# Kernel optimization log

Measured on AMD Instinct MI355X. Metric: run time of the kernel, lower is better.

The kernel has to match this reference:

```python
import jax, jax.numpy as jnp
import numpy as np
import math

EMBED_DIM = 128
SCALE = math.sqrt(EMBED_DIM)


def setup_inputs() -> dict:
    key = jax.random.key(0)
    # x: [B, N, D, L] = [4, 16, 128, 2048]
    x = jax.random.normal(key, (4, 16, 128, 2048), dtype=jnp.float32)
    return {"x": x}


def reference(x):
    # x: [B, N, D, L] -> [B, N, L, D]
    xt = jnp.swapaxes(x, -1, -2)
    # scores: [B, N, L, L] = softmax(x x^T / sqrt(D))
    scores = jnp.einsum("bnld,bnmd->bnlm", xt, xt) / jnp.asarray(SCALE, xt.dtype)
    attn = jax.nn.softmax(scores, axis=-1)
    # weighted values then mean over query positions L -> [B, N, D]
    out = jnp.einsum("bnlm,bnmd->bnld", attn, xt).mean(axis=2)
    return out
```

## Files before the change

### kernel.cpp

```cpp
#include <hip/hip_runtime.h>
#include <hip/hip_fp16.h>

#define H_  64
#define D_  128
#define L_  2048
#define RSCALE 0.08838834764831845f

typedef _Float16 half8 __attribute__((ext_vector_type(8)));
typedef float    f32x4 __attribute__((ext_vector_type(4)));

__device__ __forceinline__ void gload16(const void* g, void* l) {
    __builtin_amdgcn_global_load_lds(
        (const __attribute__((address_space(1))) void*)g,
        (__attribute__((address_space(3))) void*)l,
        16, 0, 0);
}

template <int NSW>
__device__ __forceinline__ void stage_tile(const char* __restrict__ src,
                                           char* __restrict__ dst,
                                           int wid, int lane) {
#pragma unroll
    for (int j = 0; j < NSW; ++j) {
        const unsigned o   = (unsigned)(wid * NSW + j) * 1024u + (unsigned)lane * 16u;
        const unsigned row = o >> 8;
        const unsigned so  = (o & ~255u) | ((o & 255u) ^ ((row & 7u) << 4));
        gload16(src + so, dst + (size_t)(wid * NSW + j) * 1024u);
    }
}

__global__ __launch_bounds__(256) void k_transpose(const float* __restrict__ x,
                                                   __half* __restrict__ xt) {
    const int h  = blockIdx.x;
    const int lc = blockIdx.y;
    __shared__ float raw[128][65];
    const float* xh = x + (size_t)h * D_ * L_ + (size_t)lc * 64;
    const int t = threadIdx.x;
    const int r0 = t >> 4;
    const int c4 = (t & 15) << 2;
#pragma unroll
    for (int i = 0; i < 8; ++i) {
        const int d = i * 16 + r0;
        const float4 v = *(const float4*)(xh + (size_t)d * L_ + c4);
        raw[d][c4 + 0] = v.x; raw[d][c4 + 1] = v.y;
        raw[d][c4 + 2] = v.z; raw[d][c4 + 3] = v.w;
    }
    __syncthreads();
    const int lane = t & 63, w = t >> 6;
    __half2* xth = (__half2*)(xt + (size_t)h * L_ * D_ + (size_t)lc * 64 * D_);
#pragma unroll
    for (int i = 0; i < 16; ++i) {
        const int jl = w * 16 + i;
        const float a = raw[2 * lane][jl];
        const float b = raw[2 * lane + 1][jl];
        xth[(size_t)jl * 64 + lane] = __floats2half2_rn(a, b);
    }
}

template <int PASS>
__global__ __launch_bounds__(512, 2) void k_gemm(const __half* __restrict__ xt,
                                                 const float* __restrict__ ainv,
                                                 float* __restrict__ zw) {
    __shared__ char  smA[65536];
    __shared__ char  smB[2][32768];
    __shared__ float csum[2][4][128];
    __shared__ float zfin[2][256];

    const int bid = blockIdx.x;
    const int xq  = bid >> 3;
    const int pid = xq & 3;
    const int h   = ((xq >> 2) << 3) | (bid & 7);
    const int SLOTS = (PASS == 1) ? 9 : 10;

    const int t    = threadIdx.x;
    const int lane = t & 63;
    const int wid  = t >> 6;
    const int wr   = wid >> 1;
    const int wc   = wid & 1;
    const int lo   = lane & 15, hi = lane >> 4;
    const unsigned sx = (unsigned)((lane & 7) << 4);

    const char* xh = (const char*)(xt + (size_t)h * (L_ * D_));
    float* zwh = zw + (((size_t)h * SLOTS) << 11);

#pragma unroll 1
    for (int pp = 0; pp < 2; ++pp) {
        const int p     = pp ? (7 - pid) : pid;
        const int nst   = 16 - 2 * p;
        const int rtile = 2 * p + (wr >> 1);

        stage_tile<8>(xh + (size_t)(2 * p) * 32768, smA, wid, lane);
        stage_tile<4>(xh + (size_t)(2 * p) * 32768, smB[0], wid, lane);

        float rs[4][4] = {};
        float ar[4][4];
        if (PASS == 2) {
#pragma unroll
            for (int fm = 0; fm < 4; ++fm)
#pragma unroll
                for (int r = 0; r < 4; ++r)
                    ar[fm][r] = ainv[((size_t)h << 11) + p * 256 + wr * 64 + fm * 16 + hi * 4 + r];
        }
        __syncthreads();

#pragma unroll 1
        for (int it = 0; it < nst; ++it) {
            const int ct = 2 * p + it;
            if (it + 1 < nst)
                stage_tile<4>(xh + (size_t)(ct + 1) * 32768, smB[(it + 1) & 1], wid, lane);

            float acol[4];
            if (PASS == 2) {
#pragma unroll
                for (int fn = 0; fn < 4; ++fn)
                    acol[fn] = ainv[((size_t)h << 11) + ct * 128 + wc * 64 + fn * 16 + lo];
            }

            const int rel = ct - rtile;
            float cs[4] = {0.f, 0.f, 0.f, 0.f};
            if (rel >= 0) {
                f32x4 acc[4][4] = {};
                const char* tb = smB[it & 1];
#pragma unroll
                for (int s = 0; s < 4; ++s) {
                    half8 a[4], b[4];
                    const unsigned inr = ((unsigned)(s * 64 + hi * 16)) ^ sx;
#pragma unroll
                    for (int f = 0; f < 4; ++f) {
                        a[f] = *(const half8*)(smA + (unsigned)(wr * 64 + f * 16 + lo) * 256 + inr);
                        b[f] = *(const half8*)(tb  + (unsigned)(wc * 64 + f * 16 + lo) * 256 + inr);
                    }
#pragma unroll
                    for (int fm = 0; fm < 4; ++fm)
#pragma unroll
                        for (int fn = 0; fn < 4; ++fn)
                            acc[fm][fn] = __builtin_amdgcn_mfma_f32_16x16x32_f16(
                                a[fm], b[fn], acc[fm][fn], 0, 0, 0);
                }
#pragma unroll
                for (int fm = 0; fm < 4; ++fm)
#pragma unroll
                    for (int fn = 0; fn < 4; ++fn)
#pragma unroll
                        for (int r = 0; r < 4; ++r) {
                            const float e = __expf(acc[fm][fn][r] * RSCALE);
                            if (PASS == 1) {
                                rs[fm][r] += e;
                                if (rel > 0) cs[fn] += e;
                            } else {
                                cs[fn] += ar[fm][r] * e;
                                if (rel > 0) rs[fm][r] += acol[fn] * e;
                            }
                        }
            }
#pragma unroll
            for (int fn = 0; fn < 4; ++fn) {
                cs[fn] += __shfl_xor(cs[fn], 16, 64);
                cs[fn] += __shfl_xor(cs[fn], 32, 64);
            }
            if (lane < 16) {
#pragma unroll
                for (int fn = 0; fn < 4; ++fn)
                    csum[it & 1][wr][wc * 64 + fn * 16 + lane] = cs[fn];
            }
            __syncthreads();
            if (t < 128) {
                const float su = csum[it & 1][0][t] + csum[it & 1][1][t];
                const float sl = csum[it & 1][2][t] + csum[it & 1][3][t];
                const size_t o = (size_t)ct * 128 + t;
                if (PASS == 1) {
                    zwh[((size_t)p << 11) + o] = su + sl;
                } else {
                    if (it == 0)      zwh[((size_t)9 << 11) + o] = su + sl;
                    else if (it == 1) { zwh[((size_t)p << 11) + o] = su;
                                        zwh[((size_t)9 << 11) + o] = sl; }
                    else              zwh[((size_t)p << 11) + o] = su + sl;
                }
            }
        }

#pragma unroll
        for (int fm = 0; fm < 4; ++fm)
#pragma unroll
            for (int r = 0; r < 4; ++r) {
                float v = rs[fm][r];
                v += __shfl_xor(v, 1, 64);
                v += __shfl_xor(v, 2, 64);
                v += __shfl_xor(v, 4, 64);
                v += __shfl_xor(v, 8, 64);
                if (lo == 0) zfin[wc][wr * 64 + fm * 16 + hi * 4 + r] = v;
            }
        __syncthreads();
        if (t < 256)
            zwh[((size_t)8 << 11) + p * 256 + t] = zfin[0][t] + zfin[1][t];
        __syncthreads();
    }
}

__global__ __launch_bounds__(256) void k_reduceZ(const float* __restrict__ zp,
                                                 float* __restrict__ ainv) {
    const int i = blockIdx.x * 256 + threadIdx.x;
    const int h = i >> 11, l = i & 2047, q = l >> 7;
    float z = zp[(((size_t)h * 9 + 8) << 11) + l];
#pragma unroll
    for (int p = 0; p < 8; ++p)
        if (2 * p < q) z += zp[(((size_t)h * 9 + p) << 11) + l];
    ainv[i] = 1.0f / z;
}

__global__ __launch_bounds__(256) void k_out(const float* __restrict__ x,
                                             const float* __restrict__ wp,
                                             float* __restrict__ out) {
    __shared__ float wl[L_];
    const int h = blockIdx.x >> 2, qb = blockIdx.x & 3;
    const int t = threadIdx.x, lane = t & 63, wid = t >> 6;
    for (int c = t; c < L_; c += 256) {
        const int q = c >> 7;
        float s = wp[(((size_t)h * 10 + 8) << 11) + c]
                + wp[(((size_t)h * 10 + 9) << 11) + c];
#pragma unroll
        for (int p = 0; p < 8; ++p)
            if (2 * p < q) s += wp[(((size_t)h * 10 + p) << 11) + c];
        wl[c] = s;
    }
    __syncthreads();
#pragma unroll 1
    for (int it = 0; it < 8; ++it) {
        const int d = qb * 32 + wid * 8 + it;
        const float* xr = x + ((size_t)h * D_ + d) * L_;
        float s = 0.0f;
#pragma unroll
        for (int kk = 0; kk < 8; ++kk) {
            const int m = kk * 256 + lane * 4;
            const float4 xv = *(const float4*)(xr + m);
            const float4 wv = *(const float4*)(wl + m);
            s += xv.x * wv.x + xv.y * wv.y + xv.z * wv.z + xv.w * wv.w;
        }
#pragma unroll
        for (int dm = 1; dm < 64; dm <<= 1) s += __shfl_xor(s, dm, 64);
        if (lane == 0) out[(size_t)h * D_ + d] = s * (1.0f / (float)L_);
    }
}

extern "C" void kernel_launch(void* const* d_in, const int* in_sizes, int n_in,
                              void* d_out, int out_size, void* d_ws, size_t ws_size,
                              hipStream_t stream) {
    const float* x = (const float*)d_in[0];
    float* out = (float*)d_out;
    char* ws = (char*)d_ws;

    __half* xt  = (__half*)(ws);
    float* zwp  = (float*)(ws + 33554432);
    float* ainv = (float*)(ws + 33554432 + 5242880);

    k_transpose<<<dim3(H_, L_ / 64), 256, 0, stream>>>(x, xt);
    k_gemm<1><<<256, 512, 0, stream>>>(xt, ainv, zwp);
    k_reduceZ<<<(H_ * L_) / 256, 256, 0, stream>>>(zwp, ainv);
    k_gemm<2><<<256, 512, 0, stream>>>(xt, ainv, zwp);
    k_out<<<H_ * 4, 256, 0, stream>>>(x, zwp, out);
}
```

Baseline: 170.2 us.

## Shrink GEMM tiles to 128x128, fold softmax scale into fp16 transpose, use exp2

The symmetric-score GEMM kernels now use 128-row stripes with 256-thread blocks and twice as many blocks, which removes the wasted lower-triangle half-tiles of the 256-row scheme. The 1/sqrt(D)·log2(e) factor is applied per element during the fp16 transpose so the epilogue can use a raw exp2 instead of a scaled exp. MFMA sections get raised wave priority, and the partial-sum workspace grows to 17 slots per head. The column tile is now single-buffered with a barrier per step, which drops the previous load/compute overlap. Pre-scaling before the fp16 cast also changes rounding slightly.

```diff
diff --git a/kernel.cpp b/kernel.cpp
--- a/kernel.cpp
+++ b/kernel.cpp
@@ -4,10 +4,18 @@
 #define H_  64
 #define D_  128
 #define L_  2048
-#define RSCALE 0.08838834764831845f
+#define PRE 0.35709578f
 
 typedef _Float16 half8 __attribute__((ext_vector_type(8)));
 typedef float    f32x4 __attribute__((ext_vector_type(4)));
+
+__device__ __forceinline__ float fast_exp2(float x) {
+#if __has_builtin(__builtin_amdgcn_exp2f)
+    return __builtin_amdgcn_exp2f(x);
+#else
+    return __builtin_exp2f(x);
+#endif
+}
 
 __device__ __forceinline__ void gload16(const void* g, void* l) {
     __builtin_amdgcn_global_load_lds(
@@ -16,16 +24,15 @@
         16, 0, 0);
 }
 
-template <int NSW>
-__device__ __forceinline__ void stage_tile(const char* __restrict__ src,
-                                           char* __restrict__ dst,
-                                           int wid, int lane) {
-#pragma unroll
-    for (int j = 0; j < NSW; ++j) {
-        const unsigned o   = (unsigned)(wid * NSW + j) * 1024u + (unsigned)lane * 16u;
+__device__ __forceinline__ void stage32k(const char* __restrict__ src,
+                                         char* __restrict__ dst,
+                                         int wid, int lane) {
+#pragma unroll
+    for (int j = 0; j < 8; ++j) {
+        const unsigned o   = (unsigned)(wid * 8 + j) * 1024u + (unsigned)lane * 16u;
         const unsigned row = o >> 8;
         const unsigned so  = (o & ~255u) | ((o & 255u) ^ ((row & 7u) << 4));
-        gload16(src + so, dst + (size_t)(wid * NSW + j) * 1024u);
+        gload16(src + so, dst + (size_t)(wid * 8 + j) * 1024u);
     }
 }
 
@@ -51,46 +58,44 @@
 #pragma unroll
     for (int i = 0; i < 16; ++i) {
         const int jl = w * 16 + i;
-        const float a = raw[2 * lane][jl];
-        const float b = raw[2 * lane + 1][jl];
+        const float a = raw[2 * lane][jl] * PRE;
+        const float b = raw[2 * lane + 1][jl] * PRE;
         xth[(size_t)jl * 64 + lane] = __floats2half2_rn(a, b);
     }
 }
 
 template <int PASS>
-__global__ __launch_bounds__(512, 2) void k_gemm(const __half* __restrict__ xt,
+__global__ __launch_bounds__(256, 2) void k_gemm(const __half* __restrict__ xt,
                                                  const float* __restrict__ ainv,
                                                  float* __restrict__ zw) {
-    __shared__ char  smA[65536];
-    __shared__ char  smB[2][32768];
-    __shared__ float csum[2][4][128];
-    __shared__ float zfin[2][256];
+    __shared__ char  smA[32768];
+    __shared__ char  smB[32768];
+    __shared__ float csum[2][128];
+    __shared__ float zfin[2][128];
 
     const int bid = blockIdx.x;
-    const int xq  = bid >> 3;
-    const int pid = xq & 3;
-    const int h   = ((xq >> 2) << 3) | (bid & 7);
-    const int SLOTS = (PASS == 1) ? 9 : 10;
+    const int res = bid & 7;
+    const int j   = bid >> 3;
+    const int h   = ((j >> 3) << 3) | res;
+    const int pid = j & 7;
 
     const int t    = threadIdx.x;
     const int lane = t & 63;
     const int wid  = t >> 6;
-    const int wr   = wid >> 1;
-    const int wc   = wid & 1;
+    const int wr   = wid >> 1, wc = wid & 1;
     const int lo   = lane & 15, hi = lane >> 4;
     const unsigned sx = (unsigned)((lane & 7) << 4);
 
-    const char* xh = (const char*)(xt + (size_t)h * (L_ * D_));
-    float* zwh = zw + (((size_t)h * SLOTS) << 11);
+    const char*  xh  = (const char*)(xt + (size_t)h * (L_ * D_));
+    float*       zwh = zw + ((size_t)h * 17 << 11);
+    const float* ah  = ainv + ((size_t)h << 11);
 
 #pragma unroll 1
     for (int pp = 0; pp < 2; ++pp) {
-        const int p     = pp ? (7 - pid) : pid;
-        const int nst   = 16 - 2 * p;
-        const int rtile = 2 * p + (wr >> 1);
-
-        stage_tile<8>(xh + (size_t)(2 * p) * 32768, smA, wid, lane);
-        stage_tile<4>(xh + (size_t)(2 * p) * 32768, smB[0], wid, lane);
+        const int p   = pp ? (15 - pid) : pid;
+        const int nst = 16 - p;
+
+        stage32k(xh + (size_t)p * 32768, smA, wid, lane);
 
         float rs[4][4] = {};
         float ar[4][4];
@@ -99,82 +104,89 @@
             for (int fm = 0; fm < 4; ++fm)
 #pragma unroll
                 for (int r = 0; r < 4; ++r)
-                    ar[fm][r] = ainv[((size_t)h << 11) + p * 256 + wr * 64 + fm * 16 + hi * 4 + r];
+                    ar[fm][r] = ah[p * 128 + wr * 64 + fm * 16 + hi * 4 + r];
         }
         __syncthreads();
 
 #pragma unroll 1
         for (int it = 0; it < nst; ++it) {
-            const int ct = 2 * p + it;
-            if (it + 1 < nst)
-                stage_tile<4>(xh + (size_t)(ct + 1) * 32768, smB[(it + 1) & 1], wid, lane);
-
+            const int ct = p + it;
+            const char* tb;
+            if (it == 0) {
+                tb = smA;
+            } else {
+                stage32k(xh + (size_t)ct * 32768, smB, wid, lane);
+                __syncthreads();
+                tb = smB;
+            }
             float acol[4];
             if (PASS == 2) {
 #pragma unroll
                 for (int fn = 0; fn < 4; ++fn)
-                    acol[fn] = ainv[((size_t)h << 11) + ct * 128 + wc * 64 + fn * 16 + lo];
-            }
-
-            const int rel = ct - rtile;
-            float cs[4] = {0.f, 0.f, 0.f, 0.f};
-            if (rel >= 0) {
-                f32x4 acc[4][4] = {};
-                const char* tb = smB[it & 1];
-#pragma unroll
-                for (int s = 0; s < 4; ++s) {
-                    half8 a[4], b[4];
-                    const unsigned inr = ((unsigned)(s * 64 + hi * 16)) ^ sx;
-#pragma unroll
-                    for (int f = 0; f < 4; ++f) {
-                        a[f] = *(const half8*)(smA + (unsigned)(wr * 64 + f * 16 + lo) * 256 + inr);
-                        b[f] = *(const half8*)(tb  + (unsigned)(wc * 64 + f * 16 + lo) * 256 + inr);
-                    }
-#pragma unroll
-                    for (int fm = 0; fm < 4; ++fm)
-#pragma unroll
-                        for (int fn = 0; fn < 4; ++fn)
-                            acc[fm][fn] = __builtin_amdgcn_mfma_f32_16x16x32_f16(
-                                a[fm], b[fn], acc[fm][fn], 0, 0, 0);
+                    acol[fn] = ah[ct * 128 + wc * 64 + fn * 16 + lo];
+            }
+
+            f32x4 acc[4][4] = {};
+            __builtin_amdgcn_s_setprio(1);
+#pragma unroll
+            for (int s = 0; s < 4; ++s) {
+                half8 a[4], b[4];
+                const unsigned inr = ((unsigned)(s * 64 + hi * 16)) ^ sx;
+#pragma unroll
+                for (int f = 0; f < 4; ++f) {
+                    a[f] = *(const half8*)(smA + (unsigned)(wr * 64 + f * 16 + lo) * 256 + inr);
+                    b[f] = *(const half8*)(tb  + (unsigned)(wc * 64 + f * 16 + lo) * 256 + inr);
                 }
 #pragma unroll
                 for (int fm = 0; fm < 4; ++fm)
 #pragma unroll
                     for (int fn = 0; fn < 4; ++fn)
+                        acc[fm][fn] = __builtin_amdgcn_mfma_f32_16x16x32_f16(
+                            a[fm], b[fn], acc[fm][fn], 0, 0, 0);
+            }
+            __builtin_amdgcn_s_setprio(0);
+
+            if (PASS == 1 && it == 0) {
+#pragma unroll
+                for (int fm = 0; fm < 4; ++fm)
+#pragma unroll
+                    for (int fn = 0; fn < 4; ++fn)
+#pragma unroll
+                        for (int r = 0; r < 4; ++r)
+                            rs[fm][r] += fast_exp2(acc[fm][fn][r]);
+            } else {
+                float cs[4] = {0.f, 0.f, 0.f, 0.f};
+#pragma unroll
+                for (int fm = 0; fm < 4; ++fm)
+#pragma unroll
+                    for (int fn = 0; fn < 4; ++fn)
 #pragma unroll
                         for (int r = 0; r < 4; ++r) {
-                            const float e = __expf(acc[fm][fn][r] * RSCALE);
+                            const float e = fast_exp2(acc[fm][fn][r]);
                             if (PASS == 1) {
                                 rs[fm][r] += e;
-                                if (rel > 0) cs[fn] += e;
+                                cs[fn]    += e;
                             } else {
                                 cs[fn] += ar[fm][r] * e;
-                                if (rel > 0) rs[fm][r] += acol[fn] * e;
+                                if (it > 0) rs[fm][r] += acol[fn] * e;
                             }
                         }
-            }
-#pragma unroll
-            for (int fn = 0; fn < 4; ++fn) {
-                cs[fn] += __shfl_xor(cs[fn], 16, 64);
-                cs[fn] += __shfl_xor(cs[fn], 32, 64);
-            }
-            if (lane < 16) {
-#pragma unroll
-                for (int fn = 0; fn < 4; ++fn)
-                    csum[it & 1][wr][wc * 64 + fn * 16 + lane] = cs[fn];
-            }
-            __syncthreads();
-            if (t < 128) {
-                const float su = csum[it & 1][0][t] + csum[it & 1][1][t];
-                const float sl = csum[it & 1][2][t] + csum[it & 1][3][t];
-                const size_t o = (size_t)ct * 128 + t;
-                if (PASS == 1) {
-                    zwh[((size_t)p << 11) + o] = su + sl;
-                } else {
-                    if (it == 0)      zwh[((size_t)9 << 11) + o] = su + sl;
-                    else if (it == 1) { zwh[((size_t)p << 11) + o] = su;
-                                        zwh[((size_t)9 << 11) + o] = sl; }
-                    else              zwh[((size_t)p << 11) + o] = su + sl;
+#pragma unroll
+                for (int fn = 0; fn < 4; ++fn) {
+                    cs[fn] += __shfl_xor(cs[fn], 16, 64);
+                    cs[fn] += __shfl_xor(cs[fn], 32, 64);
+                }
+                if (lane < 16) {
+#pragma unroll
+                    for (int fn = 0; fn < 4; ++fn)
+                        csum[wr][wc * 64 + fn * 16 + lane] = cs[fn];
+                }
+                __syncthreads();
+                if (t < 128) {
+                    const float s2 = csum[0][t] + csum[1][t];
+                    const size_t o = ((size_t)ct << 7) + t;
+                    if (PASS == 2 && it == 0) zwh[((size_t)16 << 11) + o] = s2;
+                    else                      zwh[((size_t)p  << 11) + o] = s2;
                 }
             }
         }
@@ -191,8 +203,8 @@
                 if (lo == 0) zfin[wc][wr * 64 + fm * 16 + hi * 4 + r] = v;
             }
         __syncthreads();
-        if (t < 256)
-            zwh[((size_t)8 << 11) + p * 256 + t] = zfin[0][t] + zfin[1][t];
+        if (t < 128)
+            zwh[((size_t)15 << 11) + ((size_t)p << 7) + t] = zfin[0][t] + zfin[1][t];
         __syncthreads();
     }
 }
@@ -201,10 +213,10 @@
                                                  float* __restrict__ ainv) {
     const int i = blockIdx.x * 256 + threadIdx.x;
     const int h = i >> 11, l = i & 2047, q = l >> 7;
-    float z = zp[(((size_t)h * 9 + 8) << 11) + l];
-#pragma unroll
-    for (int p = 0; p < 8; ++p)
-        if (2 * p < q) z += zp[(((size_t)h * 9 + p) << 11) + l];
+    float z = zp[(((size_t)h * 17 + 15) << 11) + l];
+#pragma unroll
+    for (int p = 0; p < 15; ++p)
+        if (p < q) z += zp[(((size_t)h * 17 + p) << 11) + l];
     ainv[i] = 1.0f / z;
 }
 
@@ -216,11 +228,11 @@
     const int t = threadIdx.x, lane = t & 63, wid = t >> 6;
     for (int c = t; c < L_; c += 256) {
         const int q = c >> 7;
-        float s = wp[(((size_t)h * 10 + 8) << 11) + c]
-                + wp[(((size_t)h * 10 + 9) << 11) + c];
-#pragma unroll
-        for (int p = 0; p < 8; ++p)
-            if (2 * p < q) s += wp[(((size_t)h * 10 + p) << 11) + c];
+        float s = wp[(((size_t)h * 17 + 15) << 11) + c]
+                + wp[(((size_t)h * 17 + 16) << 11) + c];
+#pragma unroll
+        for (int p = 0; p < 15; ++p)
+            if (p < q) s += wp[(((size_t)h * 17 + p) << 11) + c];
         wl[c] = s;
     }
     __syncthreads();
@@ -251,11 +263,11 @@
 
     __half* xt  = (__half*)(ws);
     float* zwp  = (float*)(ws + 33554432);
-    float* ainv = (float*)(ws + 33554432 + 5242880);
+    float* ainv = (float*)(ws + 33554432 + 8912896);
 
     k_transpose<<<dim3(H_, L_ / 64), 256, 0, stream>>>(x, xt);
-    k_gemm<1><<<256, 512, 0, stream>>>(xt, ainv, zwp);
+    k_gemm<1><<<512, 256, 0, stream>>>(xt, ainv, zwp);
     k_reduceZ<<<(H_ * L_) / 256, 256, 0, stream>>>(zwp, ainv);
-    k_gemm<2><<<256, 512, 0, stream>>>(xt, ainv, zwp);
+    k_gemm<2><<<512, 256, 0, stream>>>(xt, ainv, zwp);
     k_out<<<H_ * 4, 256, 0, stream>>>(x, zwp, out);
 }
```

Result: faster. 158.0 us (-7.1%).
